# Performance work log

Hardware: AMD Instinct MI355X
Metric: run time of the kernel (lower is better)

The kernel has to match this reference:

```python
import jax, jax.numpy as jnp
from jax import lax
import numpy as np

# Dims matching init_kwargs / input_specs
B, R, C, CIN, COUT, W, CT = 8, 96, 64, 8, 64, 8, 4


def setup_inputs() -> dict:
    key = jax.random.key(0)
    ks = jax.random.split(key, 16)
    s = 0.05
    n = lambda k, shp: s * jax.random.normal(k, shp, jnp.float32)
    return {
        "x": jax.random.normal(ks[0], (B, R, C, CIN, 1), jnp.float32),
        "x_mark": jax.random.normal(ks[1], (B, R, C, CIN, CT), jnp.float32),
        # hidden_MLP_data: Conv1d(c_in -> c_in*c_out, k=W, groups=c_in) -> per-group in=1
        "Wd": n(ks[2], (CIN * COUT, 1, W)),
        "bd": n(ks[3], (CIN * COUT,)),
        # hidden_MLP_mark: Conv1d(c_in*CT -> c_in*c_out, k=W, groups=c_in) -> per-group in=CT
        "Wm": n(ks[4], (CIN * COUT, CT, W)),
        "bm": n(ks[5], (CIN * COUT,)),
        # gate_data: k=1 grouped conv, per-group 1 -> 2*c_out; stored einsum-friendly [g, 2*c_out]
        "Gd": n(ks[6], (CIN, 2 * COUT)),
        "bgd": n(ks[7], (CIN, 2 * COUT)),
        # gate_mark: per-group CT -> 2*c_out
        "Gm": n(ks[8], (CIN, 2 * COUT, CT)),
        "bgm": n(ks[9], (CIN, 2 * COUT)),
        # gate_hid: per-group c_out -> 2*c_out
        "Gh": n(ks[10], (CIN, 2 * COUT, COUT)),
        "bgh": n(ks[11], (CIN, 2 * COUT)),
        # fc: Conv1d(c_in*c_out -> c_in*c_out, k=seq_R, groups=c_in) -> [g, o, i, R]
        "Fw": n(ks[12], (CIN, COUT, COUT, R)),
        "bf": n(ks[13], (CIN, COUT)),
    }


def _grouped_conv1d(xa, w, b, groups):
    # xa: [N, Cin, L], w: [Cout, Cin//groups, K]
    y = lax.conv_general_dilated(
        xa, w, window_strides=(1,), padding="VALID",
        dimension_numbers=("NCH", "OIH", "NCH"), feature_group_count=groups)
    return y + b[None, :, None]


def reference(x, x_mark, Wd, bd, Wm, bm, Gd, bgd, Gm, bgm, Gh, bgh, Fw, bf):
    Bv, Rv, Cv, cin, _ = x.shape
    ct = x_mark.shape[-1]
    cout = Gh.shape[-1]
    Wk = Wd.shape[-1]

    # ---- deal(): causal windowed grouped conv over R ----
    # pad W zeros in front along R, drop last step -> length R+W-1, VALID conv k=W -> R
    xz = jnp.concatenate([jnp.zeros((Bv, Wk, Cv, cin, 1), x.dtype), x], axis=1)
    xa = xz.transpose(0, 2, 3, 4, 1).reshape(Bv * Cv, cin, Rv + Wk)[:, :, :-1]
    Hd = _grouped_conv1d(xa, Wd, bd, cin)  # [B*C, cin*cout, R]

    mz = jnp.concatenate([jnp.zeros((Bv, Wk, Cv, cin, ct), x.dtype), x_mark], axis=1)
    ma = mz.transpose(0, 2, 3, 4, 1).reshape(Bv * Cv, cin * ct, Rv + Wk)[:, :, :-1]
    Hm = _grouped_conv1d(ma, Wm, bm, cin)

    hid = (Hd + Hm).reshape(Bv, Cv, cin, cout, Rv).transpose(0, 4, 1, 2, 3)  # [B,R,C,cin,cout]

    # ---- gated_unit(): kernel-1 grouped convs == per-group matmuls ----
    xs = x[..., 0]  # [B,R,C,cin]
    g = jnp.einsum("brcg,go->brcgo", xs, Gd) + bgd
    g = g + jnp.einsum("brcgt,got->brcgo", x_mark, Gm) + bgm
    g = g + jnp.einsum("brcgi,goi->brcgo", hid, Gh) + bgh
    sg = jax.nn.sigmoid(g[..., :cout])
    tg = jnp.tanh(g[..., cout:])
    hid = hid * sg + (1.0 - sg) * tg  # [B,R,C,cin,cout]

    # ---- fc: grouped conv with kernel==R -> full contraction over (in-chan, R) ----
    out = jnp.einsum("brcgi,goir->bcgo", hid, Fw) + bf  # [B,C,cin,cout]
    return out
```

## Files before the change

kernel.cpp:

```cpp
#include <hip/hip_runtime.h>
#include <hip/hip_bf16.h>

namespace {

typedef __attribute__((ext_vector_type(8))) short bh8;
typedef __attribute__((ext_vector_type(4))) short sh4;
typedef __attribute__((ext_vector_type(4))) float fx4;

constexpr int Rn = 96, Cn = 64, CINn = 8, COUTn = 64;
constexpr int NPOS = 8 * 96 * 64 * 8;
constexpr int PPG  = 8 * 96 * 64;
constexpr size_t FEAT_OFF = 0;
constexpr size_t FWT_OFF  = (size_t)NPOS * 16;
constexpr size_t CA_OFF   = FWT_OFF + (size_t)NPOS * 16;
constexpr size_t GT_OFF   = CA_OFF + 65536;
constexpr size_t PART_OFF = GT_OFF + 163840;

__device__ inline ushort f2b(float f) {
  __hip_bfloat16 h = __float2bfloat16(f);
  return __builtin_bit_cast(ushort, h);
}
__device__ inline int swz8(int bc, int rr, int ib) {
  return (bc * 1024 + rr * 128 + ib) ^ (((rr + bc) & 7) << 4);
}

#define MFMA16(a, b, c) __builtin_amdgcn_mfma_f32_16x16x32_bf16((a), (b), (c), 0, 0, 0)

__global__ __launch_bounds__(512)
void prep_k(const float* __restrict__ x, const float* __restrict__ xm,
            const float* __restrict__ Fw,
            const float* __restrict__ Gd, const float* __restrict__ bgd,
            const float* __restrict__ Gm, const float* __restrict__ bgm,
            const float* __restrict__ Gh, const float* __restrict__ bgh,
            const float* __restrict__ Wd, const float* __restrict__ bd,
            const float* __restrict__ Wm, const float* __restrict__ bm,
            ushort* __restrict__ feat, ushort* __restrict__ FwT,
            ushort* __restrict__ GT, ushort* __restrict__ cA)
{
  __shared__ float tile[64 * 97];
  const int bid = blockIdx.x, t = threadIdx.x;
  if (bid < 768) {
    const int pos = bid * 512 + t;
    const float xs = x[pos];
    const fx4 m = *(const fx4*)(xm + (size_t)pos * 4);
    bh8 o;
    o[0] = (short)f2b(xs);
    o[1] = (short)f2b(m[0]); o[2] = (short)f2b(m[1]);
    o[3] = (short)f2b(m[2]); o[4] = (short)f2b(m[3]);
    o[5] = (short)0x3F80; o[6] = 0; o[7] = 0;
    const int g = pos & 7, pb = pos >> 3;
    *(bh8*)(feat + ((size_t)g * PPG + pb) * 8) = o;
  } else if (bid < 1280) {
    const int go = bid - 768;
    const float* src = Fw + (size_t)go * 6144;
    ushort* dst = FwT + (size_t)go * 6144;
#pragma unroll
    for (int it = 0; it < 12; ++it) {
      const int idx = t + it * 512;
      tile[(idx / 96) * 97 + (idx % 96)] = src[idx];
    }
    __syncthreads();
#pragma unroll
    for (int it = 0; it < 12; ++it) {
      const int idx = t + it * 512;
      const int r = idx >> 6, i = idx & 63;
      dst[idx] = f2b(tile[i * 97 + r]);
    }
  } else if (bid < 1440) {
    const int idx = (bid - 1280) * 512 + t;
    const int ro = idx / 80, c = idx - ro * 80;
    float v = 0.f;
    if (c < 64)       v = Gh[(size_t)ro * 64 + c];
    else if (c == 64) v = Gd[ro];
    else if (c <= 68) v = Gm[(size_t)ro * 4 + (c - 65)];
    else if (c == 69) v = bgd[ro] + bgm[ro] + bgh[ro];
    GT[idx] = f2b(v);
  } else {
    const int e = (bid - 1440) * 512 + t;
    const int g = e >> 12, co = (e >> 6) & 63, k = e & 63;
    const int tap = k >> 3, tch = k & 7;
    float v = 0.f;
    if (tch == 0)      v = Wd[(g * 64 + co) * 8 + tap];
    else if (tch <= 4) v = Wm[((g * 64 + co) * 4 + (tch - 1)) * 8 + tap];
    else if (tch == 5 && tap == 0) v = bd[g * 64 + co] + bm[g * 64 + co];
    cA[e] = f2b(v);
  }
}

__global__ __launch_bounds__(512, 2)
void fused_v9(const ushort* __restrict__ feat, const ushort* __restrict__ FwT,
              const ushort* __restrict__ cA, const ushort* __restrict__ GT,
              float* __restrict__ part)
{
  __shared__ __align__(16) ushort sTabG[8 * 3 * 64 * 8];
  __shared__ __align__(16) char sHid[16384];
  __shared__ __align__(16) char sGat[2][16384];
  __shared__ float sRed[4 * 256];

  const int t    = threadIdx.x;
  const int lane = t & 63;
  const int w    = t >> 6;
  const int il   = lane >> 4;
  const int mr   = lane & 15;
  const int bid  = blockIdx.x;
  const int g    = bid & 7;
  const int bcT  = (bid >> 3) & 31;
  const int chh  = bid >> 8;
  const ushort* fg = feat + (size_t)g * PPG * 8;
  const int s4   = w & 3, hf = w >> 2;

  const int pglob = w * 16 + mr;
  const int cbcl = pglob >> 3, crr = pglob & 7;
  const int cbcg = bcT * 16 + cbcl;
  const int cbb = cbcg >> 6, ccc = cbcg & 63;
  const size_t prow = (size_t)(cbb * 96) * 64 + ccc;

  {
    const ushort* brow = GT + ((size_t)g * 128 + w * 16 + mr) * 80;
    const int xo = (il == 0) ? 64 : 72;
    *(bh8*)&sTabG[((w * 3 + 0) * 64 + lane) * 8] = *(const bh8*)(brow + 8 * il);
    *(bh8*)&sTabG[((w * 3 + 1) * 64 + lane) * 8] = *(const bh8*)(brow + 32 + 8 * il);
    *(bh8*)&sTabG[((w * 3 + 2) * 64 + lane) * 8] = *(const bh8*)(brow + xo);
  }

  bh8 aC[4][2];
  {
    const ushort* cAg = cA + g * 4096;
#pragma unroll
    for (int s = 0; s < 4; ++s)
#pragma unroll
      for (int hh = 0; hh < 2; ++hh)
        aC[s][hh] = *(const bh8*)(cAg + (s * 16 + mr) * 64 + hh * 32 + 8 * il);
  }

  const ushort* fbase = FwT + ((size_t)(g * 64 + s4 * 16 + mr) * 96) * 64 + 32 * hf + 8 * il;
  fx4 facc = {0.f, 0.f, 0.f, 0.f};
  const bh8 zpad = {0, 0, 0, 0, 0, (short)0x3F80, 0, 0};

  bh8 b0, b1, bx;
  {
    const int r0 = chh * 48;
    const int q0 = r0 + crr - 8 + il;
    const int q1 = q0 + 4;
    b0 = *(const bh8*)(fg + (prow + (size_t)(q0 > 0 ? q0 : 0) * 64) * 8);
    b1 = *(const bh8*)(fg + (prow + (size_t)(q1 > 0 ? q1 : 0) * 64) * 8);
    bx = *(const bh8*)(fg + (prow + (size_t)(r0 + crr) * 64) * 8);
  }
  __syncthreads();

#pragma unroll 1
  for (int k = 0; k < 6; ++k) {
    const int r0 = chh * 48 + k * 8;

    if (k == 0 && chh == 0) {
      const int q0 = crr - 8 + il;
      if (q0 < 0) b0 = zpad;
      if (q0 + 4 < 0) b1 = zpad;
    }
    fx4 ah[4];
#pragma unroll
    for (int s = 0; s < 4; ++s) {
      fx4 a = {0.f, 0.f, 0.f, 0.f};
      a = MFMA16(aC[s][0], b0, a);
      a = MFMA16(aC[s][1], b1, a);
      ah[s] = a;
      sh4 o4;
#pragma unroll
      for (int cc = 0; cc < 4; ++cc) o4[cc] = (short)f2b(a[cc]);
      *(sh4*)(sHid + swz8(cbcl, crr, s * 32 + il * 8)) = o4;
    }
    bh8 b0n = b0, b1n = b1, bxn = bx;
    if (k < 5) {
      const int qn0 = r0 + crr + il;
      b0n = *(const bh8*)(fg + (prow + (size_t)qn0 * 64) * 8);
      b1n = *(const bh8*)(fg + (prow + (size_t)(qn0 + 4) * 64) * 8);
      bxn = *(const bh8*)(fg + (prow + (size_t)(r0 + 8 + crr) * 64) * 8);
    }

    {
      const bh8 h0 = *(const bh8*)(sHid + swz8(cbcl, crr, 16 * il));
      const bh8 h1 = *(const bh8*)(sHid + swz8(cbcl, crr, 64 + 16 * il));
      char* gbuf = sGat[k & 1];
#pragma unroll
      for (int s = 0; s < 4; ++s) {
        fx4 accS = {0.f,0.f,0.f,0.f}, accT = {0.f,0.f,0.f,0.f};
        {
          const bh8 a0 = *(const bh8*)&sTabG[((s * 3 + 0) * 64 + lane) * 8];
          const bh8 a1 = *(const bh8*)&sTabG[((s * 3 + 1) * 64 + lane) * 8];
          const bh8 a2 = *(const bh8*)&sTabG[((s * 3 + 2) * 64 + lane) * 8];
          accS = MFMA16(a0, h0, accS);
          accS = MFMA16(a1, h1, accS);
          accS = MFMA16(a2, bx, accS);
        }
        {
          const bh8 a0 = *(const bh8*)&sTabG[(((s + 4) * 3 + 0) * 64 + lane) * 8];
          const bh8 a1 = *(const bh8*)&sTabG[(((s + 4) * 3 + 1) * 64 + lane) * 8];
          const bh8 a2 = *(const bh8*)&sTabG[(((s + 4) * 3 + 2) * 64 + lane) * 8];
          accT = MFMA16(a0, h0, accT);
          accT = MFMA16(a1, h1, accT);
          accT = MFMA16(a2, bx, accT);
        }
        sh4 o4;
#pragma unroll
        for (int cc = 0; cc < 4; ++cc) {
          const float sig = 1.f / (1.f + __expf(-accS[cc]));
          const float th  = 1.f - 2.f / (1.f + __expf(2.f * accT[cc]));
          const float h   = fmaf(sig, ah[s][cc] - th, th);
          o4[cc] = (short)f2b(h);
        }
        *(sh4*)(gbuf + swz8(cbcl, crr, s * 32 + il * 8)) = o4;
      }
    }
    __syncthreads();

    {
      const char* gbuf = sGat[k & 1];
      const ushort* fb = fbase + (size_t)r0 * 64;
#pragma unroll
      for (int f = 0; f < 8; ++f) {
        const bh8 aF = *(const bh8*)(fb + f * 64);
        const bh8 bF = *(const bh8*)(gbuf + swz8(mr, f, 64 * hf + 16 * il));
        facc = MFMA16(aF, bF, facc);
      }
    }
    b0 = b0n; b1 = b1n; bx = bxn;
  }

  if (hf == 1) {
#pragma unroll
    for (int cc = 0; cc < 4; ++cc)
      sRed[s4 * 256 + (4 * il + cc) * 16 + mr] = facc[cc];
  }
  __syncthreads();
  if (hf == 0) {
    float* pp = part + ((size_t)(chh * 8 + g) * 32 + bcT) * 1024;
#pragma unroll
    for (int cc = 0; cc < 4; ++cc)
      pp[mr * 64 + s4 * 16 + 4 * il + cc] = facc[cc] + sRed[s4 * 256 + (4 * il + cc) * 16 + mr];
  }
}

__global__ __launch_bounds__(256)
void reduce_k(const float* __restrict__ part, const float* __restrict__ bf,
              float* __restrict__ out)
{
  const int e = blockIdx.x * 256 + threadIdx.x;
  const int o = e & 63, g = (e >> 6) & 7, bcg = e >> 9;
  const int bcT = bcg >> 4, bcl = bcg & 15;
  const float s = bf[g * 64 + o]
      + part[((size_t)(0 * 8 + g) * 32 + bcT) * 1024 + bcl * 64 + o]
      + part[((size_t)(1 * 8 + g) * 32 + bcT) * 1024 + bcl * 64 + o];
  out[e] = s;
}

}

extern "C" void kernel_launch(void* const* d_in, const int* in_sizes, int n_in,
                              void* d_out, int out_size, void* d_ws, size_t ws_size,
                              hipStream_t stream) {
  const float* x   = (const float*)d_in[0];
  const float* xm  = (const float*)d_in[1];
  const float* Wd  = (const float*)d_in[2];
  const float* bd  = (const float*)d_in[3];
  const float* Wm  = (const float*)d_in[4];
  const float* bm  = (const float*)d_in[5];
  const float* Gd  = (const float*)d_in[6];
  const float* bgd = (const float*)d_in[7];
  const float* Gm  = (const float*)d_in[8];
  const float* bgm = (const float*)d_in[9];
  const float* Gh  = (const float*)d_in[10];
  const float* bgh = (const float*)d_in[11];
  const float* Fw  = (const float*)d_in[12];
  const float* bf  = (const float*)d_in[13];
  float* outp = (float*)d_out;

  ushort* feat = (ushort*)((char*)d_ws + FEAT_OFF);
  ushort* FwT  = (ushort*)((char*)d_ws + FWT_OFF);
  ushort* cA   = (ushort*)((char*)d_ws + CA_OFF);
  ushort* GT   = (ushort*)((char*)d_ws + GT_OFF);
  float*  part = (float*)((char*)d_ws + PART_OFF);

  prep_k<<<dim3(1504), dim3(512), 0, stream>>>(
      x, xm, Fw, Gd, bgd, Gm, bgm, Gh, bgh, Wd, bd, Wm, bm, feat, FwT, GT, cA);
  fused_v9<<<dim3(512), dim3(512), 0, stream>>>(feat, FwT, cA, GT, part);
  reduce_k<<<dim3(1024), dim3(256), 0, stream>>>(part, bf, outp);
}
```

Measured before the change: 56.00 us.

## Fold gate-hidden weights into conv weights to skip hid bf16 LDS round-trip

Precomputes Gh·(conv weights) in a new gwk kernel so the gate pre-activations come straight from the raw features with MFMA, without first writing hid to shared memory and reading it back. It also prescales the gate weights by log2e so sigmoid and tanh use exp2 and a hardware reciprocal, and it moves the conv A-operands from registers into LDS. This removes one LDS write/read stage per iteration and some register pressure. In exchange it adds an extra kernel launch and changes the rounding (the gate no longer sees the bf16-rounded hid).

```diff
diff --git a/kernel.cpp b/kernel.cpp
--- a/kernel.cpp
+++ b/kernel.cpp
@@ -1,5 +1,6 @@
 #include <hip/hip_runtime.h>
 #include <hip/hip_bf16.h>
+#include <math.h>
 
 namespace {
 
@@ -10,11 +11,13 @@
 constexpr int Rn = 96, Cn = 64, CINn = 8, COUTn = 64;
 constexpr int NPOS = 8 * 96 * 64 * 8;
 constexpr int PPG  = 8 * 96 * 64;
+constexpr float NLOG2E = -1.4426950408889634f;
+constexpr float LOG2E2 =  2.8853900817779268f;
 constexpr size_t FEAT_OFF = 0;
 constexpr size_t FWT_OFF  = (size_t)NPOS * 16;
 constexpr size_t CA_OFF   = FWT_OFF + (size_t)NPOS * 16;
-constexpr size_t GT_OFF   = CA_OFF + 65536;
-constexpr size_t PART_OFF = GT_OFF + 163840;
+constexpr size_t GWT_OFF  = CA_OFF + 65536;
+constexpr size_t PART_OFF = GWT_OFF + 196608;
 
 __device__ inline ushort f2b(float f) {
   __hip_bfloat16 h = __float2bfloat16(f);
@@ -31,11 +34,11 @@
             const float* __restrict__ Fw,
             const float* __restrict__ Gd, const float* __restrict__ bgd,
             const float* __restrict__ Gm, const float* __restrict__ bgm,
-            const float* __restrict__ Gh, const float* __restrict__ bgh,
+            const float* __restrict__ bgh,
             const float* __restrict__ Wd, const float* __restrict__ bd,
             const float* __restrict__ Wm, const float* __restrict__ bm,
             ushort* __restrict__ feat, ushort* __restrict__ FwT,
-            ushort* __restrict__ GT, ushort* __restrict__ cA)
+            ushort* __restrict__ GWT, ushort* __restrict__ cA)
 {
   __shared__ float tile[64 * 97];
   const int bid = blockIdx.x, t = threadIdx.x;
@@ -66,17 +69,21 @@
       const int r = idx >> 6, i = idx & 63;
       dst[idx] = f2b(tile[i * 97 + r]);
     }
-  } else if (bid < 1440) {
-    const int idx = (bid - 1280) * 512 + t;
-    const int ro = idx / 80, c = idx - ro * 80;
+  } else if (bid < 1344) {
+    const int e = (bid - 1280) * 512 + t;
+    const int j = e & 7, lp = (e >> 3) & 63, sub = (e >> 9) & 7, g = e >> 12;
+    const int il = lp >> 4, mr = lp & 15;
+    const int o2 = (sub >> 2) * 64 + (sub & 3) * 16 + mr;
     float v = 0.f;
-    if (c < 64)       v = Gh[(size_t)ro * 64 + c];
-    else if (c == 64) v = Gd[ro];
-    else if (c <= 68) v = Gm[(size_t)ro * 4 + (c - 65)];
-    else if (c == 69) v = bgd[ro] + bgm[ro] + bgh[ro];
-    GT[idx] = f2b(v);
+    if (il == 0) {
+      if (j == 0)      v = Gd[g * 128 + o2];
+      else if (j <= 4) v = Gm[(size_t)(g * 128 + o2) * 4 + (j - 1)];
+      else if (j == 5) v = bgd[g * 128 + o2] + bgm[g * 128 + o2] + bgh[g * 128 + o2];
+    }
+    v *= (sub >= 4) ? LOG2E2 : NLOG2E;
+    GWT[((size_t)(g * 24 + sub * 3 + 2) * 64 + lp) * 8 + j] = f2b(v);
   } else {
-    const int e = (bid - 1440) * 512 + t;
+    const int e = (bid - 1344) * 512 + t;
     const int g = e >> 12, co = (e >> 6) & 63, k = e & 63;
     const int tap = k >> 3, tch = k & 7;
     float v = 0.f;
@@ -87,15 +94,43 @@
   }
 }
 
+__global__ __launch_bounds__(256)
+void gwk(const float* __restrict__ Gh, const float* __restrict__ Wd,
+         const float* __restrict__ Wm, const float* __restrict__ bd,
+         const float* __restrict__ bm, ushort* __restrict__ GWT)
+{
+  const int row = blockIdx.x * 4 + (threadIdx.x >> 6);
+  const int k = threadIdx.x & 63;
+  const int g = row >> 7, o2 = row & 127;
+  const int tap = k >> 3, tch = k & 7;
+  const float* pA; int sA = 0; float mA = 0.f, mB = 0.f;
+  const float* pB;
+  if (tch == 0)      { pA = Wd + (size_t)(g * 64) * 8 + tap; sA = 8;  mA = 1.f; }
+  else if (tch <= 4) { pA = Wm + ((size_t)(g * 64) * 4 + (tch - 1)) * 8 + tap; sA = 32; mA = 1.f; }
+  else if (tch == 5 && tap == 0) { pA = bd + g * 64; sA = 1; mA = 1.f; mB = 1.f; }
+  else               { pA = Wd; }
+  pB = (mB != 0.f) ? (bm + g * 64) : pA;
+  const float* gh = Gh + (size_t)(g * 128 + o2) * 64;
+  float acc = 0.f;
+#pragma unroll 8
+  for (int i = 0; i < 64; ++i) {
+    const float wv = fmaf(mB, pB[i], mA * pA[i * sA]);
+    acc = fmaf(gh[i], wv, acc);
+  }
+  acc *= (o2 >= 64) ? LOG2E2 : NLOG2E;
+  const int half = o2 >> 6, s = (o2 >> 4) & 3, mr = o2 & 15;
+  const int sub = half * 4 + s, fs = k >> 5, lp = ((k & 31) >> 3) * 16 + mr, j = k & 7;
+  GWT[((size_t)(g * 24 + sub * 3 + fs) * 64 + lp) * 8 + j] = f2b(acc);
+}
+
 __global__ __launch_bounds__(512, 2)
-void fused_v9(const ushort* __restrict__ feat, const ushort* __restrict__ FwT,
-              const ushort* __restrict__ cA, const ushort* __restrict__ GT,
-              float* __restrict__ part)
+void fused_v10(const ushort* __restrict__ feat, const ushort* __restrict__ FwT,
+               const ushort* __restrict__ cA, const ushort* __restrict__ GWT,
+               float* __restrict__ part)
 {
-  __shared__ __align__(16) ushort sTabG[8 * 3 * 64 * 8];
-  __shared__ __align__(16) char sHid[16384];
+  __shared__ __align__(16) ushort sTab[16384];
   __shared__ __align__(16) char sGat[2][16384];
-  __shared__ float sRed[4 * 256];
+  __shared__ float sRed[1024];
 
   const int t    = threadIdx.x;
   const int lane = t & 63;
@@ -108,6 +143,7 @@
   const int chh  = bid >> 8;
   const ushort* fg = feat + (size_t)g * PPG * 8;
   const int s4   = w & 3, hf = w >> 2;
+  const int tb   = lane * 8;
 
   const int pglob = w * 16 + mr;
   const int cbcl = pglob >> 3, crr = pglob & 7;
@@ -115,25 +151,22 @@
   const int cbb = cbcg >> 6, ccc = cbcg & 63;
   const size_t prow = (size_t)(cbb * 96) * 64 + ccc;
 
+  *(bh8*)&sTab[w * 512 + tb] =
+      *(const bh8*)(cA + g * 4096 + ((w >> 1) * 16 + mr) * 64 + (w & 1) * 32 + il * 8);
   {
-    const ushort* brow = GT + ((size_t)g * 128 + w * 16 + mr) * 80;
-    const int xo = (il == 0) ? 64 : 72;
-    *(bh8*)&sTabG[((w * 3 + 0) * 64 + lane) * 8] = *(const bh8*)(brow + 8 * il);
-    *(bh8*)&sTabG[((w * 3 + 1) * 64 + lane) * 8] = *(const bh8*)(brow + 32 + 8 * il);
-    *(bh8*)&sTabG[((w * 3 + 2) * 64 + lane) * 8] = *(const bh8*)(brow + xo);
-  }
-
-  bh8 aC[4][2];
-  {
-    const ushort* cAg = cA + g * 4096;
-#pragma unroll
-    for (int s = 0; s < 4; ++s)
-#pragma unroll
-      for (int hh = 0; hh < 2; ++hh)
-        aC[s][hh] = *(const bh8*)(cAg + (s * 16 + mr) * 64 + hh * 32 + 8 * il);
-  }
-
-  const ushort* fbase = FwT + ((size_t)(g * 64 + s4 * 16 + mr) * 96) * 64 + 32 * hf + 8 * il;
+    const ushort* gsrc = GWT + (size_t)g * 12288;
+#pragma unroll
+    for (int it = 0; it < 3; ++it) {
+      const int idx = it * 512 + t;
+      *(bh8*)&sTab[4096 + idx * 8] = *(const bh8*)(gsrc + idx * 8);
+    }
+  }
+
+  int wadr[4];
+#pragma unroll
+  for (int s = 0; s < 4; ++s) wadr[s] = swz8(cbcl, crr, s * 32 + il * 8);
+  const ushort* fb0 = FwT + ((size_t)(g * 64 + s4 * 16 + mr) * 96) * 64 + 32 * hf + 8 * il;
+
   fx4 facc = {0.f, 0.f, 0.f, 0.f};
   const bh8 zpad = {0, 0, 0, 0, 0, (short)0x3F80, 0, 0};
 
@@ -149,73 +182,58 @@
   __syncthreads();
 
 #pragma unroll 1
-  for (int k = 0; k < 6; ++k) {
-    const int r0 = chh * 48 + k * 8;
-
-    if (k == 0 && chh == 0) {
-      const int q0 = crr - 8 + il;
-      if (q0 < 0) b0 = zpad;
-      if (q0 + 4 < 0) b1 = zpad;
-    }
+  for (int k6 = 0; k6 < 6; ++k6) {
+    const int r0 = chh * 48 + k6 * 8;
+    if (k6 == 0 && chh == 0) {
+      if (crr - 8 + il < 0) b0 = zpad;
+      if (crr - 4 + il < 0) b1 = zpad;
+    }
+
     fx4 ah[4];
 #pragma unroll
     for (int s = 0; s < 4; ++s) {
+      const bh8 a0 = *(const bh8*)&sTab[(s * 2 + 0) * 512 + tb];
+      const bh8 a1 = *(const bh8*)&sTab[(s * 2 + 1) * 512 + tb];
       fx4 a = {0.f, 0.f, 0.f, 0.f};
-      a = MFMA16(aC[s][0], b0, a);
-      a = MFMA16(aC[s][1], b1, a);
+      a = MFMA16(a0, b0, a);
+      a = MFMA16(a1, b1, a);
       ah[s] = a;
+    }
+
+    bh8 b0n = b0, b1n = b1, bxn = bx;
+    if (k6 < 5) {
+      const int qn = r0 + crr + il;
+      b0n = *(const bh8*)(fg + (prow + (size_t)qn * 64) * 8);
+      b1n = *(const bh8*)(fg + (prow + (size_t)(qn + 4) * 64) * 8);
+      bxn = *(const bh8*)(fg + (prow + (size_t)(r0 + 8 + crr) * 64) * 8);
+    }
+
+    char* gbuf = sGat[k6 & 1];
+#pragma unroll
+    for (int s = 0; s < 4; ++s) {
+      const int bs = (8 + s * 3) * 512 + tb;
+      const int bt = (8 + (4 + s) * 3) * 512 + tb;
+      fx4 aS = {0.f,0.f,0.f,0.f}, aT = {0.f,0.f,0.f,0.f};
+      aS = MFMA16(*(const bh8*)&sTab[bs],        b0, aS);
+      aS = MFMA16(*(const bh8*)&sTab[bs + 512],  b1, aS);
+      aS = MFMA16(*(const bh8*)&sTab[bs + 1024], bx, aS);
+      aT = MFMA16(*(const bh8*)&sTab[bt],        b0, aT);
+      aT = MFMA16(*(const bh8*)&sTab[bt + 512],  b1, aT);
+      aT = MFMA16(*(const bh8*)&sTab[bt + 1024], bx, aT);
       sh4 o4;
 #pragma unroll
-      for (int cc = 0; cc < 4; ++cc) o4[cc] = (short)f2b(a[cc]);
-      *(sh4*)(sHid + swz8(cbcl, crr, s * 32 + il * 8)) = o4;
-    }
-    bh8 b0n = b0, b1n = b1, bxn = bx;
-    if (k < 5) {
-      const int qn0 = r0 + crr + il;
-      b0n = *(const bh8*)(fg + (prow + (size_t)qn0 * 64) * 8);
-      b1n = *(const bh8*)(fg + (prow + (size_t)(qn0 + 4) * 64) * 8);
-      bxn = *(const bh8*)(fg + (prow + (size_t)(r0 + 8 + crr) * 64) * 8);
-    }
+      for (int cc = 0; cc < 4; ++cc) {
+        const float sig = __builtin_amdgcn_rcpf(1.f + exp2f(aS[cc]));
+        const float y   = exp2f(aT[cc]);
+        const float th  = (y - 1.f) * __builtin_amdgcn_rcpf(y + 1.f);
+        o4[cc] = (short)f2b(fmaf(sig, ah[s][cc] - th, th));
+      }
+      *(sh4*)(gbuf + wadr[s]) = o4;
+    }
+    __syncthreads();
 
     {
-      const bh8 h0 = *(const bh8*)(sHid + swz8(cbcl, crr, 16 * il));
-      const bh8 h1 = *(const bh8*)(sHid + swz8(cbcl, crr, 64 + 16 * il));
-      char* gbuf = sGat[k & 1];
-#pragma unroll
-      for (int s = 0; s < 4; ++s) {
-        fx4 accS = {0.f,0.f,0.f,0.f}, accT = {0.f,0.f,0.f,0.f};
-        {
-          const bh8 a0 = *(const bh8*)&sTabG[((s * 3 + 0) * 64 + lane) * 8];
-          const bh8 a1 = *(const bh8*)&sTabG[((s * 3 + 1) * 64 + lane) * 8];
-          const bh8 a2 = *(const bh8*)&sTabG[((s * 3 + 2) * 64 + lane) * 8];
-          accS = MFMA16(a0, h0, accS);
-          accS = MFMA16(a1, h1, accS);
-          accS = MFMA16(a2, bx, accS);
-        }
-        {
-          const bh8 a0 = *(const bh8*)&sTabG[(((s + 4) * 3 + 0) * 64 + lane) * 8];
-          const bh8 a1 = *(const bh8*)&sTabG[(((s + 4) * 3 + 1) * 64 + lane) * 8];
-          const bh8 a2 = *(const bh8*)&sTabG[(((s + 4) * 3 + 2) * 64 + lane) * 8];
-          accT = MFMA16(a0, h0, accT);
-          accT = MFMA16(a1, h1, accT);
-          accT = MFMA16(a2, bx, accT);
-        }
-        sh4 o4;
-#pragma unroll
-        for (int cc = 0; cc < 4; ++cc) {
-          const float sig = 1.f / (1.f + __expf(-accS[cc]));
-          const float th  = 1.f - 2.f / (1.f + __expf(2.f * accT[cc]));
-          const float h   = fmaf(sig, ah[s][cc] - th, th);
-          o4[cc] = (short)f2b(h);
-        }
-        *(sh4*)(gbuf + swz8(cbcl, crr, s * 32 + il * 8)) = o4;
-      }
-    }
-    __syncthreads();
-
-    {
-      const char* gbuf = sGat[k & 1];
-      const ushort* fb = fbase + (size_t)r0 * 64;
+      const ushort* fb = fb0 + (size_t)r0 * 64;
 #pragma unroll
       for (int f = 0; f < 8; ++f) {
         const bh8 aF = *(const bh8*)(fb + f * 64);
@@ -277,11 +295,12 @@
   ushort* feat = (ushort*)((char*)d_ws + FEAT_OFF);
   ushort* FwT  = (ushort*)((char*)d_ws + FWT_OFF);
   ushort* cA   = (ushort*)((char*)d_ws + CA_OFF);
-  ushort* GT   = (ushort*)((char*)d_ws + GT_OFF);
+  ushort* GWT  = (ushort*)((char*)d_ws + GWT_OFF);
   float*  part = (float*)((char*)d_ws + PART_OFF);
 
-  prep_k<<<dim3(1504), dim3(512), 0, stream>>>(
-      x, xm, Fw, Gd, bgd, Gm, bgm, Gh, bgh, Wd, bd, Wm, bm, feat, FwT, GT, cA);
-  fused_v9<<<dim3(512), dim3(512), 0, stream>>>(feat, FwT, cA, GT, part);
+  prep_k<<<dim3(1408), dim3(512), 0, stream>>>(
+      x, xm, Fw, Gd, bgd, Gm, bgm, bgh, Wd, bd, Wm, bm, feat, FwT, GWT, cA);
+  gwk<<<dim3(256), dim3(256), 0, stream>>>(Gh, Wd, Wm, bd, bm, GWT);
+  fused_v10<<<dim3(512), dim3(512), 0, stream>>>(feat, FwT, cA, GWT, part);
   reduce_k<<<dim3(1024), dim3(256), 0, stream>>>(part, bf, outp);
 }
```

Result: slower. 57.61 us (+2.9%).
